# Performance work log

Hardware: AMD Instinct MI355X
Metric: run time of the kernel (lower is better)

Reference implementation:

```python
import jax, jax.numpy as jnp
import numpy as np

B, N, M, U = 8, 4096, 2048, 4096
IMG = 640.0
NUM_CLASSES = 81  # COCO-like, class 0 = person


def _make_boxes(key, shape2d):
    """Valid xyxy boxes: x2>x1, y2>y1, inside a IMGxIMG canvas."""
    k1, k2 = jax.random.split(key)
    xy = jax.random.uniform(k1, shape2d + (2,), dtype=jnp.float32) * (IMG * 0.8)
    wh = jax.random.uniform(k2, shape2d + (2,), dtype=jnp.float32) * (IMG * 0.2) + 1.0
    return jnp.concatenate([xy, xy + wh], axis=-1)


def setup_inputs() -> dict:
    key = jax.random.key(0)
    ks = jax.random.split(key, 8)
    pred_boxes = _make_boxes(ks[0], (B, N))
    gt_boxes = _make_boxes(ks[1], (B, M))
    gt_valid = jax.random.uniform(ks[2], (B, M)) < 0.9
    gt_boxes = jnp.where(gt_valid[..., None], gt_boxes, 0.0)
    pred_scores = jax.random.uniform(ks[3], (B, N), dtype=jnp.float32)
    pred_classes = jax.random.randint(ks[4], (B, N), 0, NUM_CLASSES, dtype=jnp.int32)
    union_scores = jax.random.uniform(ks[5], (U,), dtype=jnp.float32)
    union_classes = jax.random.randint(ks[6], (U,), 0, NUM_CLASSES, dtype=jnp.int32)
    return {
        "pred_boxes": pred_boxes,
        "pred_scores": pred_scores,
        "pred_classes": pred_classes,
        "gt_boxes": gt_boxes,
        "union_scores": union_scores,
        "union_classes": union_classes,
    }


def reference(pred_boxes, pred_scores, pred_classes, gt_boxes, union_scores, union_classes):
    # --- fused pairwise IoU, replacing the per-box python loop ---
    p = pred_boxes[:, :, None, :]   # [B, N, 1, 4]
    g = gt_boxes[:, None, :, :]     # [B, 1, M, 4]
    iw = jnp.maximum(jnp.minimum(p[..., 2], g[..., 2]) - jnp.maximum(p[..., 0], g[..., 0]), 0.0)
    ih = jnp.maximum(jnp.minimum(p[..., 3], g[..., 3]) - jnp.maximum(p[..., 1], g[..., 1]), 0.0)
    inters = iw * ih                # [B, N, M]
    area_p = (p[..., 2] - p[..., 0]) * (p[..., 3] - p[..., 1])
    area_g = (g[..., 2] - g[..., 0]) * (g[..., 3] - g[..., 1])
    uni = area_p + area_g - inters
    iou = inters / jnp.maximum(uni, 1e-9)

    # preds filtered to people class (==0); gt rows with zero sum filtered out
    pred_is_person = pred_classes == 0                       # [B, N]
    gt_valid = jnp.sum(gt_boxes, axis=-1) != 0               # [B, M]
    pair_mask = pred_is_person[:, :, None] & gt_valid[:, None, :]
    iou = jnp.where(pair_mask, iou, 0.0)

    iou_max = jnp.max(iou, axis=(1, 2))                      # [B]
    # max_iou_t[i] set only when people_scores non-empty
    has_person = jnp.any(pred_is_person, axis=1)
    iou_max = jnp.where(has_person, iou_max, 0.0)
    max_iou_t = jnp.mean(iou_max)

    # union-image detection: max score among person detections
    max_prob_t = jnp.max(jnp.where(union_classes == 0, union_scores, -jnp.inf))

    return jnp.stack([max_prob_t, max_iou_t])
```

## Files before the change

kernel.cpp:

```cpp
#include <hip/hip_runtime.h>
#include <math.h>

#define BATCH  8
#define NPRED  4096
#define MGT    2048
#define UU     4096
#define SPB    8
#define NPROD  (BATCH * SPB)
#define PSLICE (NPRED / SPB)
#define WREG   (PSLICE / 4)
#define GPT    (MGT / 256)
#define MAGIC  0xC0FFEE00u
#define STRIDE 16

__global__ __launch_bounds__(256) void fused_kernel(
    const float4* __restrict__ pred_boxes,
    const int2*   __restrict__ pred_classes2,
    const float4* __restrict__ gt_boxes,
    const float4* __restrict__ union_scores4,
    const int4*   __restrict__ union_classes4,
    unsigned long long* __restrict__ slots,
    float* __restrict__ out)
{
    const int tid = threadIdx.x;
    const int blk = blockIdx.x;

    if (blk < NPROD) {
        __shared__ float4 plist[4][WREG];
        __shared__ float  parea[4][WREG];
        __shared__ int    lcnt[4];

        const int w    = tid >> 6;
        const int lane = tid & 63;
        const int b    = blk >> 3;
        const int psub = blk & 7;

        const int  cbase = b * (NPRED / 2) + psub * (PSLICE / 2) + tid;
        const int2 cl    = pred_classes2[cbase];
        const float4 bx0 = pred_boxes[cbase * 2 + 0];
        const float4 bx1 = pred_boxes[cbase * 2 + 1];

        float4 g[GPT];
        #pragma unroll
        for (int k = 0; k < GPT; ++k)
            g[k] = gt_boxes[b * MGT + k * 256 + tid];

        float ga[GPT];
        #pragma unroll
        for (int k = 0; k < GPT; ++k)
            ga[k] = (g[k].z - g[k].x) * (g[k].w - g[k].y);

        if (lane == 0) lcnt[w] = 0;
        if (cl.x == 0) { int p = atomicAdd(&lcnt[w], 1); plist[w][p] = bx0; parea[w][p] = (bx0.z - bx0.x) * (bx0.w - bx0.y); }
        if (cl.y == 0) { int p = atomicAdd(&lcnt[w], 1); plist[w][p] = bx1; parea[w][p] = (bx1.z - bx1.x) * (bx1.w - bx1.y); }
        __syncthreads();

        float best[GPT];
        #pragma unroll
        for (int k = 0; k < GPT; ++k) best[k] = 0.0f;

        #pragma unroll
        for (int ww = 0; ww < 4; ++ww) {
            const int cnt = lcnt[ww];
            for (int j = 0; j < cnt; ++j) {
                const float4 p  = plist[ww][j];
                const float  ap = parea[ww][j];
                #pragma unroll
                for (int k = 0; k < GPT; ++k) {
                    float iw = fminf(p.z, g[k].z) - fmaxf(p.x, g[k].x);
                    float ih = fminf(p.w, g[k].w) - fmaxf(p.y, g[k].y);
                    iw = fmaxf(iw, 0.0f); ih = fmaxf(ih, 0.0f);
                    const float inter = iw * ih;
                    const float uni   = ap + ga[k] - inter;
                    best[k] = fmaxf(best[k], inter * __builtin_amdgcn_rcpf(fmaxf(uni, 1e-9f)));
                }
            }
        }

        float bestv = best[0];
        #pragma unroll
        for (int k = 1; k < GPT; ++k) bestv = fmaxf(bestv, best[k]);

        #pragma unroll
        for (int off = 32; off >= 1; off >>= 1)
            bestv = fmaxf(bestv, __shfl_xor(bestv, off));
        if (lane == 0) {
            const unsigned long long v =
                ((unsigned long long)MAGIC << 32) | (unsigned long long)__float_as_uint(bestv);
            __hip_atomic_store(&slots[(w * 64 + blk) * STRIDE], v,
                               __ATOMIC_RELAXED, __HIP_MEMORY_SCOPE_AGENT);
        }
    } else {
        __shared__ float pmax[4];
        float mp = -INFINITY;
        #pragma unroll
        for (int s = 0; s < UU / (256 * 4); ++s) {
            const int i = s * 256 + tid;
            const int4   c = union_classes4[i];
            const float4 v = union_scores4[i];
            if (c.x == 0) mp = fmaxf(mp, v.x);
            if (c.y == 0) mp = fmaxf(mp, v.y);
            if (c.z == 0) mp = fmaxf(mp, v.z);
            if (c.w == 0) mp = fmaxf(mp, v.w);
        }
        #pragma unroll
        for (int off = 32; off >= 1; off >>= 1)
            mp = fmaxf(mp, __shfl_xor(mp, off));
        if ((tid & 63) == 0) pmax[tid >> 6] = mp;
        __syncthreads();
        if (tid == 0)
            out[0] = fmaxf(fmaxf(pmax[0], pmax[1]), fmaxf(pmax[2], pmax[3]));

        if (tid < 64) {
            unsigned long long v0, v1, v2, v3;
            do {
                v0 = __hip_atomic_load(&slots[(0 * 64 + tid) * STRIDE], __ATOMIC_RELAXED, __HIP_MEMORY_SCOPE_AGENT);
                v1 = __hip_atomic_load(&slots[(1 * 64 + tid) * STRIDE], __ATOMIC_RELAXED, __HIP_MEMORY_SCOPE_AGENT);
                v2 = __hip_atomic_load(&slots[(2 * 64 + tid) * STRIDE], __ATOMIC_RELAXED, __HIP_MEMORY_SCOPE_AGENT);
                v3 = __hip_atomic_load(&slots[(3 * 64 + tid) * STRIDE], __ATOMIC_RELAXED, __HIP_MEMORY_SCOPE_AGENT);
            } while (((unsigned int)(v0 >> 32) != MAGIC) || ((unsigned int)(v1 >> 32) != MAGIC) ||
                     ((unsigned int)(v2 >> 32) != MAGIC) || ((unsigned int)(v3 >> 32) != MAGIC));
            __hip_atomic_store(&slots[(0 * 64 + tid) * STRIDE], 0ULL, __ATOMIC_RELAXED, __HIP_MEMORY_SCOPE_AGENT);
            __hip_atomic_store(&slots[(1 * 64 + tid) * STRIDE], 0ULL, __ATOMIC_RELAXED, __HIP_MEMORY_SCOPE_AGENT);
            __hip_atomic_store(&slots[(2 * 64 + tid) * STRIDE], 0ULL, __ATOMIC_RELAXED, __HIP_MEMORY_SCOPE_AGENT);
            __hip_atomic_store(&slots[(3 * 64 + tid) * STRIDE], 0ULL, __ATOMIC_RELAXED, __HIP_MEMORY_SCOPE_AGENT);

            unsigned int q = max(max((unsigned int)v0, (unsigned int)v1),
                                 max((unsigned int)v2, (unsigned int)v3));
            q = max(q, (unsigned int)__shfl_xor((int)q, 1, 8));
            q = max(q, (unsigned int)__shfl_xor((int)q, 2, 8));
            q = max(q, (unsigned int)__shfl_xor((int)q, 4, 8));
            float s = 0.0f;
            #pragma unroll
            for (int i = 0; i < 8; ++i)
                s += __uint_as_float((unsigned int)__shfl((int)q, 8 * i, 64));
            if (tid == 0)
                out[1] = s * 0.125f;
        }
    }
}

extern "C" void kernel_launch(void* const* d_in, const int* in_sizes, int n_in,
                              void* d_out, int out_size, void* d_ws, size_t ws_size,
                              hipStream_t stream) {
    const float4* pred_boxes    = (const float4*)d_in[0];
    const int2*   pred_classes2 = (const int2*)d_in[2];
    const float4* gt_boxes      = (const float4*)d_in[3];
    const float4* union_scores4 = (const float4*)d_in[4];
    const int4*   union_classes4= (const int4*)d_in[5];
    float* out = (float*)d_out;
    unsigned long long* slots = (unsigned long long*)d_ws;

    fused_kernel<<<NPROD + 1, 256, 0, stream>>>(pred_boxes, pred_classes2, gt_boxes,
                                                union_scores4, union_classes4, slots, out);
}
```

Before: 11.58 us.

## Replace spin-waiting reducer block with a publish-and-check finish in every block

The dedicated extra block that spin-polled per-wave slots is removed. Each producer block now reduces its four wave maxima in shared memory and publishes one slot. It then waits for its own store, reads all 64 slots once, and if every slot carries the magic tag it writes both outputs and clears the slots. Every block also redundantly recomputes the union person-score max, so no separate block is needed for it. The aim is to drop the polling loop and the extra block's latency, at the cost of duplicated small union loads and a relaxed-ordering completion check that relies on the vmcnt wait for correctness.

```diff
diff --git a/kernel.cpp b/kernel.cpp
--- a/kernel.cpp
+++ b/kernel.cpp
@@ -22,111 +22,108 @@
     unsigned long long* __restrict__ slots,
     float* __restrict__ out)
 {
-    const int tid = threadIdx.x;
-    const int blk = blockIdx.x;
+    __shared__ float4 plist[4][WREG];
+    __shared__ float  parea[4][WREG];
+    __shared__ int    lcnt[4];
+    __shared__ float  wmax[4];
+    __shared__ float  umax[4];
 
-    if (blk < NPROD) {
-        __shared__ float4 plist[4][WREG];
-        __shared__ float  parea[4][WREG];
-        __shared__ int    lcnt[4];
+    const int tid  = threadIdx.x;
+    const int blk  = blockIdx.x;
+    const int w    = tid >> 6;
+    const int lane = tid & 63;
+    const int b    = blk >> 3;
+    const int psub = blk & 7;
 
-        const int w    = tid >> 6;
-        const int lane = tid & 63;
-        const int b    = blk >> 3;
-        const int psub = blk & 7;
+    const int  cbase = b * (NPRED / 2) + psub * (PSLICE / 2) + tid;
+    const int2 cl    = pred_classes2[cbase];
+    const float4 bx0 = pred_boxes[cbase * 2 + 0];
+    const float4 bx1 = pred_boxes[cbase * 2 + 1];
 
-        const int  cbase = b * (NPRED / 2) + psub * (PSLICE / 2) + tid;
-        const int2 cl    = pred_classes2[cbase];
-        const float4 bx0 = pred_boxes[cbase * 2 + 0];
-        const float4 bx1 = pred_boxes[cbase * 2 + 1];
+    float4 g[GPT];
+    #pragma unroll
+    for (int k = 0; k < GPT; ++k)
+        g[k] = gt_boxes[b * MGT + k * 256 + tid];
 
-        float4 g[GPT];
-        #pragma unroll
-        for (int k = 0; k < GPT; ++k)
-            g[k] = gt_boxes[b * MGT + k * 256 + tid];
+    int4   uc[4];
+    float4 us[4];
+    #pragma unroll
+    for (int s = 0; s < 4; ++s) {
+        uc[s] = union_classes4[s * 256 + tid];
+        us[s] = union_scores4[s * 256 + tid];
+    }
 
-        float ga[GPT];
-        #pragma unroll
-        for (int k = 0; k < GPT; ++k)
-            ga[k] = (g[k].z - g[k].x) * (g[k].w - g[k].y);
+    float ga[GPT];
+    #pragma unroll
+    for (int k = 0; k < GPT; ++k)
+        ga[k] = (g[k].z - g[k].x) * (g[k].w - g[k].y);
 
-        if (lane == 0) lcnt[w] = 0;
-        if (cl.x == 0) { int p = atomicAdd(&lcnt[w], 1); plist[w][p] = bx0; parea[w][p] = (bx0.z - bx0.x) * (bx0.w - bx0.y); }
-        if (cl.y == 0) { int p = atomicAdd(&lcnt[w], 1); plist[w][p] = bx1; parea[w][p] = (bx1.z - bx1.x) * (bx1.w - bx1.y); }
-        __syncthreads();
+    if (lane == 0) lcnt[w] = 0;
+    if (cl.x == 0) { int p = atomicAdd(&lcnt[w], 1); plist[w][p] = bx0; parea[w][p] = (bx0.z - bx0.x) * (bx0.w - bx0.y); }
+    if (cl.y == 0) { int p = atomicAdd(&lcnt[w], 1); plist[w][p] = bx1; parea[w][p] = (bx1.z - bx1.x) * (bx1.w - bx1.y); }
+    __syncthreads();
 
-        float best[GPT];
-        #pragma unroll
-        for (int k = 0; k < GPT; ++k) best[k] = 0.0f;
+    float best[GPT];
+    #pragma unroll
+    for (int k = 0; k < GPT; ++k) best[k] = 0.0f;
 
-        #pragma unroll
-        for (int ww = 0; ww < 4; ++ww) {
-            const int cnt = lcnt[ww];
-            for (int j = 0; j < cnt; ++j) {
-                const float4 p  = plist[ww][j];
-                const float  ap = parea[ww][j];
-                #pragma unroll
-                for (int k = 0; k < GPT; ++k) {
-                    float iw = fminf(p.z, g[k].z) - fmaxf(p.x, g[k].x);
-                    float ih = fminf(p.w, g[k].w) - fmaxf(p.y, g[k].y);
-                    iw = fmaxf(iw, 0.0f); ih = fmaxf(ih, 0.0f);
-                    const float inter = iw * ih;
-                    const float uni   = ap + ga[k] - inter;
-                    best[k] = fmaxf(best[k], inter * __builtin_amdgcn_rcpf(fmaxf(uni, 1e-9f)));
-                }
+    #pragma unroll
+    for (int ww = 0; ww < 4; ++ww) {
+        const int cnt = lcnt[ww];
+        for (int j = 0; j < cnt; ++j) {
+            const float4 p  = plist[ww][j];
+            const float  ap = parea[ww][j];
+            #pragma unroll
+            for (int k = 0; k < GPT; ++k) {
+                float iw = fminf(p.z, g[k].z) - fmaxf(p.x, g[k].x);
+                float ih = fminf(p.w, g[k].w) - fmaxf(p.y, g[k].y);
+                iw = fmaxf(iw, 0.0f); ih = fmaxf(ih, 0.0f);
+                const float inter = iw * ih;
+                const float uni   = ap + ga[k] - inter;
+                best[k] = fmaxf(best[k], inter * __builtin_amdgcn_rcpf(fmaxf(uni, 1e-9f)));
             }
         }
+    }
 
-        float bestv = best[0];
-        #pragma unroll
-        for (int k = 1; k < GPT; ++k) bestv = fmaxf(bestv, best[k]);
+    float bestv = best[0];
+    #pragma unroll
+    for (int k = 1; k < GPT; ++k) bestv = fmaxf(bestv, best[k]);
 
-        #pragma unroll
-        for (int off = 32; off >= 1; off >>= 1)
-            bestv = fmaxf(bestv, __shfl_xor(bestv, off));
-        if (lane == 0) {
-            const unsigned long long v =
-                ((unsigned long long)MAGIC << 32) | (unsigned long long)__float_as_uint(bestv);
-            __hip_atomic_store(&slots[(w * 64 + blk) * STRIDE], v,
+    float mp = -INFINITY;
+    #pragma unroll
+    for (int s = 0; s < 4; ++s) {
+        if (uc[s].x == 0) mp = fmaxf(mp, us[s].x);
+        if (uc[s].y == 0) mp = fmaxf(mp, us[s].y);
+        if (uc[s].z == 0) mp = fmaxf(mp, us[s].z);
+        if (uc[s].w == 0) mp = fmaxf(mp, us[s].w);
+    }
+
+    #pragma unroll
+    for (int off = 32; off >= 1; off >>= 1) {
+        bestv = fmaxf(bestv, __shfl_xor(bestv, off));
+        mp    = fmaxf(mp,    __shfl_xor(mp,    off));
+    }
+    if (lane == 0) { wmax[w] = bestv; umax[w] = mp; }
+    __syncthreads();
+
+    if (w == 0) {
+        const float bb = fmaxf(fmaxf(wmax[0], wmax[1]), fmaxf(wmax[2], wmax[3]));
+        const unsigned long long myv =
+            ((unsigned long long)MAGIC << 32) | (unsigned long long)__float_as_uint(bb);
+        if (lane == 0)
+            __hip_atomic_store(&slots[blk * STRIDE], myv,
                                __ATOMIC_RELAXED, __HIP_MEMORY_SCOPE_AGENT);
-        }
-    } else {
-        __shared__ float pmax[4];
-        float mp = -INFINITY;
-        #pragma unroll
-        for (int s = 0; s < UU / (256 * 4); ++s) {
-            const int i = s * 256 + tid;
-            const int4   c = union_classes4[i];
-            const float4 v = union_scores4[i];
-            if (c.x == 0) mp = fmaxf(mp, v.x);
-            if (c.y == 0) mp = fmaxf(mp, v.y);
-            if (c.z == 0) mp = fmaxf(mp, v.z);
-            if (c.w == 0) mp = fmaxf(mp, v.w);
-        }
-        #pragma unroll
-        for (int off = 32; off >= 1; off >>= 1)
-            mp = fmaxf(mp, __shfl_xor(mp, off));
-        if ((tid & 63) == 0) pmax[tid >> 6] = mp;
-        __syncthreads();
-        if (tid == 0)
-            out[0] = fmaxf(fmaxf(pmax[0], pmax[1]), fmaxf(pmax[2], pmax[3]));
+        const float mpb = fmaxf(fmaxf(umax[0], umax[1]), fmaxf(umax[2], umax[3]));
 
-        if (tid < 64) {
-            unsigned long long v0, v1, v2, v3;
-            do {
-                v0 = __hip_atomic_load(&slots[(0 * 64 + tid) * STRIDE], __ATOMIC_RELAXED, __HIP_MEMORY_SCOPE_AGENT);
-                v1 = __hip_atomic_load(&slots[(1 * 64 + tid) * STRIDE], __ATOMIC_RELAXED, __HIP_MEMORY_SCOPE_AGENT);
-                v2 = __hip_atomic_load(&slots[(2 * 64 + tid) * STRIDE], __ATOMIC_RELAXED, __HIP_MEMORY_SCOPE_AGENT);
-                v3 = __hip_atomic_load(&slots[(3 * 64 + tid) * STRIDE], __ATOMIC_RELAXED, __HIP_MEMORY_SCOPE_AGENT);
-            } while (((unsigned int)(v0 >> 32) != MAGIC) || ((unsigned int)(v1 >> 32) != MAGIC) ||
-                     ((unsigned int)(v2 >> 32) != MAGIC) || ((unsigned int)(v3 >> 32) != MAGIC));
-            __hip_atomic_store(&slots[(0 * 64 + tid) * STRIDE], 0ULL, __ATOMIC_RELAXED, __HIP_MEMORY_SCOPE_AGENT);
-            __hip_atomic_store(&slots[(1 * 64 + tid) * STRIDE], 0ULL, __ATOMIC_RELAXED, __HIP_MEMORY_SCOPE_AGENT);
-            __hip_atomic_store(&slots[(2 * 64 + tid) * STRIDE], 0ULL, __ATOMIC_RELAXED, __HIP_MEMORY_SCOPE_AGENT);
-            __hip_atomic_store(&slots[(3 * 64 + tid) * STRIDE], 0ULL, __ATOMIC_RELAXED, __HIP_MEMORY_SCOPE_AGENT);
+        asm volatile("s_waitcnt vmcnt(0)" ::: "memory");
 
-            unsigned int q = max(max((unsigned int)v0, (unsigned int)v1),
-                                 max((unsigned int)v2, (unsigned int)v3));
+        unsigned long long v = myv;
+        if (lane != blk)
+            v = __hip_atomic_load(&slots[lane * STRIDE],
+                                  __ATOMIC_RELAXED, __HIP_MEMORY_SCOPE_AGENT);
+
+        if (__all((unsigned int)(v >> 32) == MAGIC)) {
+            unsigned int q = (unsigned int)v;
             q = max(q, (unsigned int)__shfl_xor((int)q, 1, 8));
             q = max(q, (unsigned int)__shfl_xor((int)q, 2, 8));
             q = max(q, (unsigned int)__shfl_xor((int)q, 4, 8));
@@ -134,8 +131,12 @@
             #pragma unroll
             for (int i = 0; i < 8; ++i)
                 s += __uint_as_float((unsigned int)__shfl((int)q, 8 * i, 64));
-            if (tid == 0)
+            if (lane == 0) {
+                out[0] = mpb;
                 out[1] = s * 0.125f;
+            }
+            __hip_atomic_store(&slots[lane * STRIDE], 0ULL,
+                               __ATOMIC_RELAXED, __HIP_MEMORY_SCOPE_AGENT);
         }
     }
 }
@@ -151,6 +152,6 @@
     float* out = (float*)d_out;
     unsigned long long* slots = (unsigned long long*)d_ws;
 
-    fused_kernel<<<NPROD + 1, 256, 0, stream>>>(pred_boxes, pred_classes2, gt_boxes,
-                                                union_scores4, union_classes4, slots, out);
+    fused_kernel<<<NPROD, 256, 0, stream>>>(pred_boxes, pred_classes2, gt_boxes,
+                                            union_scores4, union_classes4, slots, out);
 }
```

Result: slower. 12.00 us (+3.6%).
